# Performance work log

Hardware: AMD Instinct MI355X
Metric: run time of the kernel (lower is better)

## Reference

```python
import jax, jax.numpy as jnp
import numpy as np
import math


def _build_lookup(S):
    # Vectorized port of build_hierarchical_index_lookup_table (static, numpy).
    L = int(math.log2(S))
    total = 2 * S - 1
    max_valid = total - 2  # root is never a neighbor
    idx = np.full((S, L), -1, dtype=np.int32)
    cmask = np.zeros((S, L), dtype=bool)
    n = np.arange(S, dtype=np.int64)
    for lvl in range(L):
        if lvl == 0:
            nn = n ^ 1
            pair = n
        else:
            pair = n // 2 + S
            nn = pair ^ 1
        valid = nn <= max_valid
        idx[:, lvl] = np.where(valid, nn.astype(np.int32), idx[:, lvl])
        cmask[:, lvl] = np.where(valid, (pair < nn) & valid, cmask[:, lvl])
        n = nn
    return jnp.asarray(idx), jnp.asarray(cmask)


def _tree_kv(k, v, levels, scale):
    # Build parent nodes bottom-up. Parent K is the mean of its two children;
    # parent V is refined by the fused parent-self attention (build_parent_nodes):
    # 3-way softmax over [self, child0, child1] with eps 1e-9 in the denominator.
    K_parts, V_parts = [k], [v]
    Kc, Vc = k, v
    for _ in range(levels):
        Kc0, Kc1 = Kc[:, 0::2], Kc[:, 1::2]
        Vc0, Vc1 = Vc[:, 0::2], Vc[:, 1::2]
        Kp = 0.5 * (Kc0 + Kc1)
        Vp = 0.5 * (Vc0 + Vc1)
        s_self = jnp.einsum('bphd,bphd->bph', Kp, Kp) * scale
        s0 = jnp.einsum('bphd,bphd->bph', Kp, Kc0) * scale
        s1 = jnp.einsum('bphd,bphd->bph', Kp, Kc1) * scale
        m = jnp.maximum(s_self, jnp.maximum(s0, s1))
        e_self = jnp.exp(s_self - m)
        e0 = jnp.exp(s0 - m)
        e1 = jnp.exp(s1 - m)
        denom = e_self + e0 + e1 + 1e-9
        Vp = (e_self[..., None] * Vp + e0[..., None] * Vc0 + e1[..., None] * Vc1) / denom[..., None]
        K_parts.append(Kp)
        V_parts.append(Vp)
        Kc, Vc = Kp, Vp
    # Full tree: leaves first, then each parent level -> [B, 2S-1, H, D]
    return jnp.concatenate(K_parts, axis=1), jnp.concatenate(V_parts, axis=1)


def setup_inputs() -> dict:
    key = jax.random.key(0)
    kq, kk, kv = jax.random.split(key, 3)
    B, S, H, D = 4, 4096, 8, 64
    q = jax.random.normal(kq, (B, S, H, D), dtype=jnp.float32)
    k = jax.random.normal(kk, (B, S, H, D), dtype=jnp.float32)
    v = jax.random.normal(kv, (B, S, H, D), dtype=jnp.float32)
    return {'q': q, 'k': k, 'v': v}


def reference(q, k, v):
    B, S, H, D = q.shape
    L = int(math.log2(S))
    scale = 1.0 / math.sqrt(D)
    idx, cmask = _build_lookup(S)          # [S, L] int32, [S, L] bool
    Kf, Vf = _tree_kv(k, v, L, scale)      # [B, 2S-1, H, D]
    kc = Kf[:, idx]                        # [B, S, L, H, D] tree-indexed gather
    vc = Vf[:, idx]
    s_self = jnp.einsum('bshd,bshd->bsh', q, k) * scale
    s_cross = jnp.einsum('bshd,bslhd->bshl', q, kc) * scale
    s_cross = jnp.where(cmask[None, :, None, :], -jnp.inf, s_cross)
    m = jnp.maximum(s_self, jnp.max(s_cross, axis=-1))  # online-softmax max
    e_self = jnp.exp(s_self - m)
    e_cross = jnp.exp(s_cross - m[..., None])
    denom = e_self + jnp.sum(e_cross, axis=-1)
    out = (e_self[..., None] * v + jnp.einsum('bshl,bslhd->bshd', e_cross, vc)) / denom[..., None]
    return out
```

## Files before the change

### kernel.cpp

```cpp
#include <hip/hip_runtime.h>


#define S 4096
#define H 8
#define D 64
#define B 4
#define NBH 32
#define NHI 254
#define SCALE 0.125f
#define ROWF 68

__device__ inline float red16(float x) {
    x += __shfl_xor(x, 1);
    x += __shfl_xor(x, 2);
    x += __shfl_xor(x, 4);
    x += __shfl_xor(x, 8);
    return x;
}

__device__ inline float dot4(const float4 a, const float4 b) {
    return a.x * b.x + a.y * b.y + a.z * b.z + a.w * b.w;
}

__device__ inline void combine(const float4 k0, const float4 k1,
                               const float4 v0, const float4 v1,
                               float4& kp, float4& vp) {
    kp.x = 0.5f * (k0.x + k1.x);
    kp.y = 0.5f * (k0.y + k1.y);
    kp.z = 0.5f * (k0.z + k1.z);
    kp.w = 0.5f * (k0.w + k1.w);
    float pss = red16(dot4(kp, kp)) * SCALE;
    float p0  = red16(dot4(kp, k0)) * SCALE;
    float p1  = red16(dot4(kp, k1)) * SCALE;
    float m  = fmaxf(pss, fmaxf(p0, p1));
    float es = __expf(pss - m), e0 = __expf(p0 - m), e1 = __expf(p1 - m);
    float inv = 1.0f / (es + e0 + e1 + 1e-9f);
    float h = 0.5f * es;
    vp.x = ((h + e0) * v0.x + (h + e1) * v1.x) * inv;
    vp.y = ((h + e0) * v0.y + (h + e1) * v1.y) * inv;
    vp.z = ((h + e0) * v0.z + (h + e1) * v1.z) * inv;
    vp.w = ((h + e0) * v0.w + (h + e1) * v1.w) * inv;
}

__global__ __launch_bounds__(256, 8) void chunk5(
    const float* __restrict__ k, const float* __restrict__ v,
    float* __restrict__ khi, float* __restrict__ vhi)
{
    __shared__ float lsk[32 * ROWF], lsv[32 * ROWF];
    const int t = threadIdx.x;
    const int sub = t & 15;
    const int pg = t >> 4;
    const int blk = blockIdx.x;
    const int pair = blk & 63;
    const int bh = blk >> 6;
    const int b = bh >> 3, h = bh & 7;
    const int csel = pg >> 3;
    const int jg = pg & 7;
    const int c = pair * 2 + csel;
    const int rowBase = csel * 16;

#pragma unroll
    for (int r = 0; r < 2; ++r) {
        int j = jg + r * 8;
        int s0 = c * 32 + 2 * j;
        size_t a0 = ((((size_t)b * S + s0) * H + h) * D) + sub * 4;
        float4 k0 = *(const float4*)(k + a0);
        float4 k1 = *(const float4*)(k + a0 + H * D);
        float4 v0 = *(const float4*)(v + a0);
        float4 v1 = *(const float4*)(v + a0 + H * D);
        float4 kp, vp;
        combine(k0, k1, v0, v1, kp, vp);
        *(float4*)(lsk + (rowBase + j) * ROWF + sub * 4) = kp;
        *(float4*)(lsv + (rowBase + j) * ROWF + sub * 4) = vp;
    }
    __syncthreads();

#pragma unroll
    for (int tt = 1; tt <= 4; ++tt) {
        int nodes = 16 >> tt;
        for (int j = jg; j < nodes; j += 8) {
            int r0 = rowBase + ((2 * j) << (tt - 1));
            int r1 = rowBase + ((2 * j + 1) << (tt - 1));
            float4 k0 = *(const float4*)(lsk + r0 * ROWF + sub * 4);
            float4 k1 = *(const float4*)(lsk + r1 * ROWF + sub * 4);
            float4 v0 = *(const float4*)(lsv + r0 * ROWF + sub * 4);
            float4 v1 = *(const float4*)(lsv + r1 * ROWF + sub * 4);
            float4 kp, vp;
            combine(k0, k1, v0, v1, kp, vp);
            if (tt < 4) {
                *(float4*)(lsk + (rowBase + (j << tt)) * ROWF + sub * 4) = kp;
                *(float4*)(lsv + (rowBase + (j << tt)) * ROWF + sub * 4) = vp;
            } else {
                size_t g = ((size_t)bh * NHI + c) * 64 + sub * 4;
                *(float4*)(khi + g) = kp;
                *(float4*)(vhi + g) = vp;
            }
        }
        __syncthreads();
    }
}

__global__ __launch_bounds__(256) void build_hi(
    float* __restrict__ khi, float* __restrict__ vhi)
{
    __shared__ float lk[128 * ROWF], lv[128 * ROWF];
    const int t = threadIdx.x;
    const int sub = t & 15;
    const int pg = t >> 4;
    const int bh = blockIdx.x;
    size_t base = (size_t)bh * NHI * 64;

    for (int i = t; i < 2048; i += 256) {
        int row = i >> 4, s16 = i & 15;
        *(float4*)(lk + row * ROWF + s16 * 4) = *(const float4*)(khi + base + i * 4);
        *(float4*)(lv + row * ROWF + s16 * 4) = *(const float4*)(vhi + base + i * 4);
    }
    __syncthreads();

#pragma unroll
    for (int tt = 1; tt <= 6; ++tt) {
        int nodes = 128 >> tt;
        int off = 256 - (256 >> tt);
        for (int j = pg; j < nodes; j += 16) {
            int r0 = (2 * j) << (tt - 1);
            int r1 = (2 * j + 1) << (tt - 1);
            float4 k0 = *(const float4*)(lk + r0 * ROWF + sub * 4);
            float4 k1 = *(const float4*)(lk + r1 * ROWF + sub * 4);
            float4 v0 = *(const float4*)(lv + r0 * ROWF + sub * 4);
            float4 v1 = *(const float4*)(lv + r1 * ROWF + sub * 4);
            float4 kp, vp;
            combine(k0, k1, v0, v1, kp, vp);
            *(float4*)(lk + (j << tt) * ROWF + sub * 4) = kp;
            *(float4*)(lv + (j << tt) * ROWF + sub * 4) = vp;
            size_t g = base + (size_t)(off + j) * 64 + sub * 4;
            *(float4*)(khi + g) = kp;
            *(float4*)(vhi + g) = vp;
        }
        __syncthreads();
    }
}

__global__ __launch_bounds__(256, 8) void attn32(
    const float* __restrict__ q, const float* __restrict__ k,
    const float* __restrict__ v,
    const float* __restrict__ khi, const float* __restrict__ vhi,
    float* __restrict__ out)
{
    __shared__ float tk[30 * ROWF], tv[30 * ROWF];
    __shared__ float pk[7 * ROWF], pv[7 * ROWF];
    const int t = threadIdx.x;
    const int sub = t & 15;
    const int pg = t >> 4;
    const int blk = blockIdx.x;
    const int c32 = blk & 127;
    const int bh = blk >> 7;
    const int b = bh >> 3, h = bh & 7;

    {
        int pl = (pg < 7) ? pg : pg - 8;
        if (pl >= 0 && pl < 7 && pg != 7 && pg != 15) {
            if ((c32 >> pl) & 1) {
                int off = 256 - (256 >> pl);
                int node = off + ((c32 >> pl) ^ 1);
                size_t a = ((size_t)bh * NHI + node) * 64 + sub * 4;
                if (pg < 7) *(float4*)(pk + pl * ROWF + sub * 4) = *(const float4*)(khi + a);
                else        *(float4*)(pv + pl * ROWF + sub * 4) = *(const float4*)(vhi + a);
            }
        }
    }

    {
        int j = pg;
        int s0 = c32 * 32 + 2 * j;
        size_t a0 = ((((size_t)b * S + s0) * H + h) * D) + sub * 4;
        float4 k0 = *(const float4*)(k + a0);
        float4 k1 = *(const float4*)(k + a0 + H * D);
        float4 v0 = *(const float4*)(v + a0);
        float4 v1 = *(const float4*)(v + a0 + H * D);
        float4 kp, vp;
        combine(k0, k1, v0, v1, kp, vp);
        *(float4*)(tk + j * ROWF + sub * 4) = kp;
        *(float4*)(tv + j * ROWF + sub * 4) = vp;
    }
    __syncthreads();
    if (pg < 8) {
        int j = pg;
        float4 k0 = *(const float4*)(tk + (2 * j) * ROWF + sub * 4);
        float4 k1 = *(const float4*)(tk + (2 * j + 1) * ROWF + sub * 4);
        float4 v0 = *(const float4*)(tv + (2 * j) * ROWF + sub * 4);
        float4 v1 = *(const float4*)(tv + (2 * j + 1) * ROWF + sub * 4);
        float4 kp, vp;
        combine(k0, k1, v0, v1, kp, vp);
        *(float4*)(tk + (16 + j) * ROWF + sub * 4) = kp;
        *(float4*)(tv + (16 + j) * ROWF + sub * 4) = vp;
    }
    __syncthreads();
    if (pg < 4) {
        int j = pg;
        float4 k0 = *(const float4*)(tk + (16 + 2 * j) * ROWF + sub * 4);
        float4 k1 = *(const float4*)(tk + (16 + 2 * j + 1) * ROWF + sub * 4);
        float4 v0 = *(const float4*)(tv + (16 + 2 * j) * ROWF + sub * 4);
        float4 v1 = *(const float4*)(tv + (16 + 2 * j + 1) * ROWF + sub * 4);
        float4 kp, vp;
        combine(k0, k1, v0, v1, kp, vp);
        *(float4*)(tk + (24 + j) * ROWF + sub * 4) = kp;
        *(float4*)(tv + (24 + j) * ROWF + sub * 4) = vp;
    }
    __syncthreads();
    if (pg < 2) {
        int j = pg;
        float4 k0 = *(const float4*)(tk + (24 + 2 * j) * ROWF + sub * 4);
        float4 k1 = *(const float4*)(tk + (24 + 2 * j + 1) * ROWF + sub * 4);
        float4 v0 = *(const float4*)(tv + (24 + 2 * j) * ROWF + sub * 4);
        float4 v1 = *(const float4*)(tv + (24 + 2 * j + 1) * ROWF + sub * 4);
        float4 kp, vp;
        combine(k0, k1, v0, v1, kp, vp);
        *(float4*)(tk + (28 + j) * ROWF + sub * 4) = kp;
        *(float4*)(tv + (28 + j) * ROWF + sub * 4) = vp;
    }
    __syncthreads();

#pragma unroll 1
    for (int r = 0; r < 2; ++r) {
        int sl = (pg >> 2) + (pg & 3) * 4 + r * 16;
        int s = c32 * 32 + sl;
        size_t qa = ((((size_t)b * S + s) * H + h) * D) + sub * 4;
        float4 q4 = *(const float4*)(q + qa);
        float4 k4 = *(const float4*)(k + qa);
        float4 v4 = *(const float4*)(v + qa);

        float ss = red16(dot4(q4, k4)) * SCALE;

        float sc[12];
        float4 vc0 = v4;
        const bool odd = (s & 1) != 0;
        if (odd) {
            float4 kc0 = *(const float4*)(k + qa - H * D);
            vc0 = *(const float4*)(v + qa - H * D);
            sc[0] = red16(dot4(q4, kc0)) * SCALE;
        } else {
            sc[0] = -1e38f;
        }
#pragma unroll
        for (int l = 1; l <= 4; ++l) {
            if ((s >> l) & 1) {
                int base = 32 - (32 >> (l - 1));
                int loc = base + (((s >> l) ^ 1) - (c32 << (5 - l)));
                float4 kc = *(const float4*)(tk + loc * ROWF + sub * 4);
                sc[l] = red16(dot4(q4, kc)) * SCALE;
            } else sc[l] = -1e38f;
        }
#pragma unroll
        for (int l = 5; l <= 11; ++l) {
            if ((c32 >> (l - 5)) & 1) {
                float4 kc = *(const float4*)(pk + (l - 5) * ROWF + sub * 4);
                sc[l] = red16(dot4(q4, kc)) * SCALE;
            } else sc[l] = -1e38f;
        }

        float m = ss;
#pragma unroll
        for (int l = 0; l < 12; ++l) m = fmaxf(m, sc[l]);

        float es = __expf(ss - m);
        float denom = es;
        float4 acc;
        acc.x = es * v4.x; acc.y = es * v4.y;
        acc.z = es * v4.z; acc.w = es * v4.w;

        if (odd) {
            float e = __expf(sc[0] - m);
            denom += e;
            acc.x += e * vc0.x; acc.y += e * vc0.y;
            acc.z += e * vc0.z; acc.w += e * vc0.w;
        }
#pragma unroll
        for (int l = 1; l <= 4; ++l) {
            if ((s >> l) & 1) {
                int base = 32 - (32 >> (l - 1));
                int loc = base + (((s >> l) ^ 1) - (c32 << (5 - l)));
                float4 vc = *(const float4*)(tv + loc * ROWF + sub * 4);
                float e = __expf(sc[l] - m);
                denom += e;
                acc.x += e * vc.x; acc.y += e * vc.y;
                acc.z += e * vc.z; acc.w += e * vc.w;
            }
        }
#pragma unroll
        for (int l = 5; l <= 11; ++l) {
            if ((c32 >> (l - 5)) & 1) {
                float4 vc = *(const float4*)(pv + (l - 5) * ROWF + sub * 4);
                float e = __expf(sc[l] - m);
                denom += e;
                acc.x += e * vc.x; acc.y += e * vc.y;
                acc.z += e * vc.z; acc.w += e * vc.w;
            }
        }
        float inv = 1.0f / denom;
        float4 o;
        o.x = acc.x * inv; o.y = acc.y * inv;
        o.z = acc.z * inv; o.w = acc.w * inv;
        *(float4*)(out + qa) = o;
    }
}

extern "C" void kernel_launch(void* const* d_in, const int* in_sizes, int n_in,
                              void* d_out, int out_size, void* d_ws, size_t ws_size,
                              hipStream_t stream) {
    const float* q = (const float*)d_in[0];
    const float* k = (const float*)d_in[1];
    const float* v = (const float*)d_in[2];
    float* outp = (float*)d_out;
    float* khi = (float*)d_ws;
    float* vhi = khi + (size_t)NBH * NHI * D;

    hipLaunchKernelGGL(chunk5, dim3(NBH * 64), dim3(256), 0, stream,
                       k, v, khi, vhi);
    hipLaunchKernelGGL(build_hi, dim3(NBH), dim3(256), 0, stream, khi, vhi);
    hipLaunchKernelGGL(attn32, dim3(NBH * 128), dim3(256), 0, stream,
                       q, k, v, khi, vhi, outp);
}
```

Measured before the change: 166.9 us.

## Fuse top-level tree build into chunk kernel via last-block atomic counter

Removes the separate build_hi launch. Each (b,h) group's last-finishing chunk block, found through an atomic counter, builds the upper tree levels directly in global memory. The attention kernel now loads its q/k/v pair once and reuses those registers for both self and sibling terms, instead of reloading per query row. It also merges the small intra-chunk tree levels under a single barrier. This adds a memset launch and serialised tail work inside the last blocks, and occupancy hints change.

```diff
diff --git a/kernel.cpp b/kernel.cpp
--- a/kernel.cpp
+++ b/kernel.cpp
@@ -42,11 +42,13 @@
     vp.w = ((h + e0) * v0.w + (h + e1) * v1.w) * inv;
 }
 
-__global__ __launch_bounds__(256, 8) void chunk5(
+__global__ __launch_bounds__(256, 8) void tree_all(
     const float* __restrict__ k, const float* __restrict__ v,
-    float* __restrict__ khi, float* __restrict__ vhi)
+    float* __restrict__ khi, float* __restrict__ vhi,
+    int* __restrict__ cnt)
 {
     __shared__ float lsk[32 * ROWF], lsv[32 * ROWF];
+    __shared__ int amLast;
     const int t = threadIdx.x;
     const int sub = t & 15;
     const int pg = t >> 4;
@@ -98,49 +100,39 @@
         }
         __syncthreads();
     }
-}
-
-__global__ __launch_bounds__(256) void build_hi(
-    float* __restrict__ khi, float* __restrict__ vhi)
-{
-    __shared__ float lk[128 * ROWF], lv[128 * ROWF];
-    const int t = threadIdx.x;
-    const int sub = t & 15;
-    const int pg = t >> 4;
-    const int bh = blockIdx.x;
+
+    if (t == 0) {
+        __threadfence();
+        int old = __hip_atomic_fetch_add(&cnt[bh], 1, __ATOMIC_ACQ_REL,
+                                         __HIP_MEMORY_SCOPE_AGENT);
+        amLast = (old == 63) ? 1 : 0;
+    }
+    __syncthreads();
+    if (!amLast) return;
+    __threadfence();
+
     size_t base = (size_t)bh * NHI * 64;
-
-    for (int i = t; i < 2048; i += 256) {
-        int row = i >> 4, s16 = i & 15;
-        *(float4*)(lk + row * ROWF + s16 * 4) = *(const float4*)(khi + base + i * 4);
-        *(float4*)(lv + row * ROWF + s16 * 4) = *(const float4*)(vhi + base + i * 4);
-    }
-    __syncthreads();
-
-#pragma unroll
-    for (int tt = 1; tt <= 6; ++tt) {
-        int nodes = 128 >> tt;
-        int off = 256 - (256 >> tt);
+    int srcO = 0;
+#pragma unroll
+    for (int lvl = 0; lvl < 6; ++lvl) {
+        int nodes = 64 >> lvl;
+        int dstO = srcO + (nodes << 1);
         for (int j = pg; j < nodes; j += 16) {
-            int r0 = (2 * j) << (tt - 1);
-            int r1 = (2 * j + 1) << (tt - 1);
-            float4 k0 = *(const float4*)(lk + r0 * ROWF + sub * 4);
-            float4 k1 = *(const float4*)(lk + r1 * ROWF + sub * 4);
-            float4 v0 = *(const float4*)(lv + r0 * ROWF + sub * 4);
-            float4 v1 = *(const float4*)(lv + r1 * ROWF + sub * 4);
+            float4 k0 = *(const float4*)(khi + base + (size_t)(srcO + 2 * j) * 64 + sub * 4);
+            float4 k1 = *(const float4*)(khi + base + (size_t)(srcO + 2 * j + 1) * 64 + sub * 4);
+            float4 v0 = *(const float4*)(vhi + base + (size_t)(srcO + 2 * j) * 64 + sub * 4);
+            float4 v1 = *(const float4*)(vhi + base + (size_t)(srcO + 2 * j + 1) * 64 + sub * 4);
             float4 kp, vp;
             combine(k0, k1, v0, v1, kp, vp);
-            *(float4*)(lk + (j << tt) * ROWF + sub * 4) = kp;
-            *(float4*)(lv + (j << tt) * ROWF + sub * 4) = vp;
-            size_t g = base + (size_t)(off + j) * 64 + sub * 4;
-            *(float4*)(khi + g) = kp;
-            *(float4*)(vhi + g) = vp;
+            *(float4*)(khi + base + (size_t)(dstO + j) * 64 + sub * 4) = kp;
+            *(float4*)(vhi + base + (size_t)(dstO + j) * 64 + sub * 4) = vp;
         }
         __syncthreads();
-    }
-}
-
-__global__ __launch_bounds__(256, 8) void attn32(
+        srcO = dstO;
+    }
+}
+
+__global__ __launch_bounds__(256, 7) void attn32(
     const float* __restrict__ q, const float* __restrict__ k,
     const float* __restrict__ v,
     const float* __restrict__ khi, const float* __restrict__ vhi,
@@ -169,78 +161,71 @@
         }
     }
 
+    const int s0 = c32 * 32 + 2 * pg;
+    const size_t a0 = ((((size_t)b * S + s0) * H + h) * D) + sub * 4;
+    const float4 k0 = *(const float4*)(k + a0);
+    const float4 k1 = *(const float4*)(k + a0 + H * D);
+    const float4 v0 = *(const float4*)(v + a0);
+    const float4 v1 = *(const float4*)(v + a0 + H * D);
+    const float4 q0 = *(const float4*)(q + a0);
+    const float4 q1 = *(const float4*)(q + a0 + H * D);
+
     {
-        int j = pg;
-        int s0 = c32 * 32 + 2 * j;
-        size_t a0 = ((((size_t)b * S + s0) * H + h) * D) + sub * 4;
-        float4 k0 = *(const float4*)(k + a0);
-        float4 k1 = *(const float4*)(k + a0 + H * D);
-        float4 v0 = *(const float4*)(v + a0);
-        float4 v1 = *(const float4*)(v + a0 + H * D);
         float4 kp, vp;
         combine(k0, k1, v0, v1, kp, vp);
-        *(float4*)(tk + j * ROWF + sub * 4) = kp;
-        *(float4*)(tv + j * ROWF + sub * 4) = vp;
+        *(float4*)(tk + pg * ROWF + sub * 4) = kp;
+        *(float4*)(tv + pg * ROWF + sub * 4) = vp;
     }
     __syncthreads();
-    if (pg < 8) {
-        int j = pg;
-        float4 k0 = *(const float4*)(tk + (2 * j) * ROWF + sub * 4);
-        float4 k1 = *(const float4*)(tk + (2 * j + 1) * ROWF + sub * 4);
-        float4 v0 = *(const float4*)(tv + (2 * j) * ROWF + sub * 4);
-        float4 v1 = *(const float4*)(tv + (2 * j + 1) * ROWF + sub * 4);
-        float4 kp, vp;
-        combine(k0, k1, v0, v1, kp, vp);
-        *(float4*)(tk + (16 + j) * ROWF + sub * 4) = kp;
-        *(float4*)(tv + (16 + j) * ROWF + sub * 4) = vp;
+
+    if (pg < 4) {
+#pragma unroll
+        for (int u = 0; u < 2; ++u) {
+            int j = 2 * pg + u;
+            float4 ka = *(const float4*)(tk + (2 * j) * ROWF + sub * 4);
+            float4 kb = *(const float4*)(tk + (2 * j + 1) * ROWF + sub * 4);
+            float4 va = *(const float4*)(tv + (2 * j) * ROWF + sub * 4);
+            float4 vb = *(const float4*)(tv + (2 * j + 1) * ROWF + sub * 4);
+            float4 kp, vp;
+            combine(ka, kb, va, vb, kp, vp);
+            *(float4*)(tk + (16 + j) * ROWF + sub * 4) = kp;
+            *(float4*)(tv + (16 + j) * ROWF + sub * 4) = vp;
+        }
+        {
+            float4 ka = *(const float4*)(tk + (16 + 2 * pg) * ROWF + sub * 4);
+            float4 kb = *(const float4*)(tk + (16 + 2 * pg + 1) * ROWF + sub * 4);
+            float4 va = *(const float4*)(tv + (16 + 2 * pg) * ROWF + sub * 4);
+            float4 vb = *(const float4*)(tv + (16 + 2 * pg + 1) * ROWF + sub * 4);
+            float4 kp, vp;
+            combine(ka, kb, va, vb, kp, vp);
+            *(float4*)(tk + (24 + pg) * ROWF + sub * 4) = kp;
+            *(float4*)(tv + (24 + pg) * ROWF + sub * 4) = vp;
+        }
+        if (pg < 2) {
+            float4 ka = *(const float4*)(tk + (24 + 2 * pg) * ROWF + sub * 4);
+            float4 kb = *(const float4*)(tk + (24 + 2 * pg + 1) * ROWF + sub * 4);
+            float4 va = *(const float4*)(tv + (24 + 2 * pg) * ROWF + sub * 4);
+            float4 vb = *(const float4*)(tv + (24 + 2 * pg + 1) * ROWF + sub * 4);
+            float4 kp, vp;
+            combine(ka, kb, va, vb, kp, vp);
+            *(float4*)(tk + (28 + pg) * ROWF + sub * 4) = kp;
+            *(float4*)(tv + (28 + pg) * ROWF + sub * 4) = vp;
+        }
     }
     __syncthreads();
-    if (pg < 4) {
-        int j = pg;
-        float4 k0 = *(const float4*)(tk + (16 + 2 * j) * ROWF + sub * 4);
-        float4 k1 = *(const float4*)(tk + (16 + 2 * j + 1) * ROWF + sub * 4);
-        float4 v0 = *(const float4*)(tv + (16 + 2 * j) * ROWF + sub * 4);
-        float4 v1 = *(const float4*)(tv + (16 + 2 * j + 1) * ROWF + sub * 4);
-        float4 kp, vp;
-        combine(k0, k1, v0, v1, kp, vp);
-        *(float4*)(tk + (24 + j) * ROWF + sub * 4) = kp;
-        *(float4*)(tv + (24 + j) * ROWF + sub * 4) = vp;
-    }
-    __syncthreads();
-    if (pg < 2) {
-        int j = pg;
-        float4 k0 = *(const float4*)(tk + (24 + 2 * j) * ROWF + sub * 4);
-        float4 k1 = *(const float4*)(tk + (24 + 2 * j + 1) * ROWF + sub * 4);
-        float4 v0 = *(const float4*)(tv + (24 + 2 * j) * ROWF + sub * 4);
-        float4 v1 = *(const float4*)(tv + (24 + 2 * j + 1) * ROWF + sub * 4);
-        float4 kp, vp;
-        combine(k0, k1, v0, v1, kp, vp);
-        *(float4*)(tk + (28 + j) * ROWF + sub * 4) = kp;
-        *(float4*)(tv + (28 + j) * ROWF + sub * 4) = vp;
-    }
-    __syncthreads();
-
-#pragma unroll 1
+
+#pragma unroll
     for (int r = 0; r < 2; ++r) {
-        int sl = (pg >> 2) + (pg & 3) * 4 + r * 16;
-        int s = c32 * 32 + sl;
-        size_t qa = ((((size_t)b * S + s) * H + h) * D) + sub * 4;
-        float4 q4 = *(const float4*)(q + qa);
-        float4 k4 = *(const float4*)(k + qa);
-        float4 v4 = *(const float4*)(v + qa);
+        const int s = s0 + r;
+        const float4 q4 = r ? q1 : q0;
+        const float4 k4 = r ? k1 : k0;
+        const float4 v4 = r ? v1 : v0;
 
         float ss = red16(dot4(q4, k4)) * SCALE;
 
         float sc[12];
-        float4 vc0 = v4;
-        const bool odd = (s & 1) != 0;
-        if (odd) {
-            float4 kc0 = *(const float4*)(k + qa - H * D);
-            vc0 = *(const float4*)(v + qa - H * D);
-            sc[0] = red16(dot4(q4, kc0)) * SCALE;
-        } else {
-            sc[0] = -1e38f;
-        }
+        if (r) sc[0] = red16(dot4(q4, k0)) * SCALE;
+        else   sc[0] = -1e38f;
 #pragma unroll
         for (int l = 1; l <= 4; ++l) {
             if ((s >> l) & 1) {
@@ -268,11 +253,11 @@
         acc.x = es * v4.x; acc.y = es * v4.y;
         acc.z = es * v4.z; acc.w = es * v4.w;
 
-        if (odd) {
+        if (r) {
             float e = __expf(sc[0] - m);
             denom += e;
-            acc.x += e * vc0.x; acc.y += e * vc0.y;
-            acc.z += e * vc0.z; acc.w += e * vc0.w;
+            acc.x += e * v0.x; acc.y += e * v0.y;
+            acc.z += e * v0.z; acc.w += e * v0.w;
         }
 #pragma unroll
         for (int l = 1; l <= 4; ++l) {
@@ -300,7 +285,7 @@
         float4 o;
         o.x = acc.x * inv; o.y = acc.y * inv;
         o.z = acc.z * inv; o.w = acc.w * inv;
-        *(float4*)(out + qa) = o;
+        *(float4*)(out + a0 + r * H * D) = o;
     }
 }
 
@@ -313,10 +298,11 @@
     float* outp = (float*)d_out;
     float* khi = (float*)d_ws;
     float* vhi = khi + (size_t)NBH * NHI * D;
-
-    hipLaunchKernelGGL(chunk5, dim3(NBH * 64), dim3(256), 0, stream,
-                       k, v, khi, vhi);
-    hipLaunchKernelGGL(build_hi, dim3(NBH), dim3(256), 0, stream, khi, vhi);
+    int* cnt = (int*)(vhi + (size_t)NBH * NHI * D);
+
+    hipMemsetAsync(cnt, 0, NBH * sizeof(int), stream);
+    hipLaunchKernelGGL(tree_all, dim3(NBH * 64), dim3(256), 0, stream,
+                       k, v, khi, vhi, cnt);
     hipLaunchKernelGGL(attn32, dim3(NBH * 128), dim3(256), 0, stream,
                        q, k, v, khi, vhi, outp);
 }
```

Measured after the change: 319.8 us. 91.7% more time.
